# Kernel tuning notes

Measured on AMD Instinct MI355X. Metric: run time of the kernel, lower is better.

## Reference

```python
import jax, jax.numpy as jnp
import numpy as np

NUM_GRAPHS = 64
N, E, H = 100000, 3200000, 64


def _glorot(k, shape):
    fan_in = shape[0]
    return jax.random.normal(k, shape, jnp.float32) * (1.0 / np.sqrt(fan_in))


def setup_inputs() -> dict:
    key = jax.random.key(0)
    ks = jax.random.split(key, 16)
    edge_index = jax.random.randint(ks[0], (2, E), 0, N)
    edge_weight = jax.random.uniform(ks[1], (E,), dtype=jnp.float32)
    batch = jnp.sort(jax.random.randint(ks[2], (N,), 0, NUM_GRAPHS))
    return {
        "edge_index": edge_index,
        "edge_weight": edge_weight,
        "batch": batch,
        "num_nodes": N,
        "W1": _glorot(ks[3], (1, H)), "b1": jnp.zeros((H,), jnp.float32),
        "W2": _glorot(ks[4], (H, H)), "b2": jnp.zeros((H,), jnp.float32),
        "W3": _glorot(ks[5], (H, H)), "b3": jnp.zeros((H,), jnp.float32),
        "W4": _glorot(ks[6], (H, H)), "b4": jnp.zeros((H,), jnp.float32),
        "W5": _glorot(ks[7], (H, H)), "b5": jnp.zeros((H,), jnp.float32),
        "lin_w": _glorot(ks[8], (H, 1)), "lin_b": jnp.zeros((1,), jnp.float32),
    }


def _gcn_layer(x, W, b, src, dst, w, n):
    # GCNConv(normalize=False): linear transform then weighted scatter-add over edges.
    h = x @ W                                  # [N, H]
    m = h[src] * w[:, None]                    # [E, H] messages
    return jax.ops.segment_sum(m, dst, num_segments=n) + b


def reference(edge_index, edge_weight, batch, num_nodes,
              W1, b1, W2, b2, W3, b3, W4, b4, W5, b5, lin_w, lin_b):
    src, dst = edge_index[0], edge_index[1]
    x = jnp.ones((num_nodes, 1), jnp.float32)
    for W, b in ((W1, b1), (W2, b2), (W3, b3), (W4, b4), (W5, b5)):
        x = jax.nn.relu(_gcn_layer(x, W, b, src, dst, edge_weight, num_nodes))
        # dropout p=0.1 is identity in eval mode
    # global mean pool per graph
    sums = jax.ops.segment_sum(x, batch, num_segments=NUM_GRAPHS)      # [G, H]
    counts = jax.ops.segment_sum(jnp.ones((num_nodes,), x.dtype), batch,
                                 num_segments=NUM_GRAPHS)
    pooled = sums / jnp.maximum(counts, 1.0)[:, None]
    return pooled @ lin_w + lin_b                                      # [G, 1]
```

## Files before the change

kernel.cpp:

```cpp
#include <hip/hip_runtime.h>

#define H 64
#define NUM_GRAPHS 64
#define BSHIFT 8
#define BSIZE 256
#define MAXNB 512
#define CHUNK 8192
#define BKT 8192
#define PADE 16
#define CSRB (BKT + BSIZE * PADE)
#define RPB 16

typedef unsigned int uint;
typedef unsigned short ushort;
typedef __attribute__((ext_vector_type(4))) float f32x4;
typedef __attribute__((ext_vector_type(8))) short short8;

__device__ __forceinline__ float bf2f(ushort u) {
    return __uint_as_float(((uint)u) << 16);
}
__device__ __forceinline__ ushort f2bf(float f) {
    uint b = __float_as_uint(f);
    b += 0x7FFFu + ((b >> 16) & 1u);
    return (ushort)(b >> 16);
}

__global__ void init_kernel(int* __restrict__ bucketCur, int NB) {
    int i = blockIdx.x * 256 + threadIdx.x;
    if (i < NB) bucketCur[i] = i * BKT;
}

__global__ __launch_bounds__(1024) void part_kernel(const int* __restrict__ src,
        const int* __restrict__ dst, const float* __restrict__ w,
        int* __restrict__ bucketCur, int2* __restrict__ bucketed, int E, int NB) {
    __shared__ int h[MAXNB];
    __shared__ int basev[MAXNB];
    __shared__ int lbase[MAXNB + 1];
    __shared__ int s[512];
    __shared__ int2 stage[CHUNK];
    int tid = threadIdx.x;
    for (int i = tid; i < NB; i += 1024) h[i] = 0;
    __syncthreads();
    int cbase = blockIdx.x * CHUNK;
    int cend = min(cbase + CHUNK, E);
    for (int e = cbase + tid; e < cend; e += 1024)
        atomicAdd(&h[dst[e] >> BSHIFT], 1);
    __syncthreads();
    for (int i = tid; i < NB; i += 1024) {
        int c = h[i];
        basev[i] = c ? atomicAdd(&bucketCur[i], c) : 0;
    }
    if (tid < 512) s[tid] = (tid < NB) ? h[tid] : 0;
    __syncthreads();
    for (int off = 1; off < 512; off <<= 1) {
        int t = (tid < 512 && tid >= off) ? s[tid - off] : 0;
        __syncthreads();
        if (tid < 512) s[tid] += t;
        __syncthreads();
    }
    if (tid < NB) lbase[tid + 1] = s[tid];
    if (tid == 0) lbase[0] = 0;
    __syncthreads();
    for (int i = tid; i < NB; i += 1024) h[i] = 0;
    __syncthreads();
    for (int e = cbase + tid; e < cend; e += 1024) {
        int d = dst[e];
        int b = d >> BSHIFT;
        int slot = atomicAdd(&h[b], 1);
        stage[lbase[b] + slot] =
            make_int2(((d & (BSIZE - 1)) << 17) | src[e], __float_as_int(w[e]));
    }
    __syncthreads();
    int lane = tid & 63, wv = tid >> 6;
    for (int b = wv; b < NB; b += 16) {
        int lb = lbase[b], cnt = lbase[b + 1] - lb, gb = basev[b];
        int lim = (b + 1) * BKT;
        for (int k = lane; k < cnt; k += 64)
            if (gb + k < lim) bucketed[gb + k] = stage[lb + k];
    }
}

__global__ __launch_bounds__(512) void bsort_kernel(const int* __restrict__ bucketCur,
        const int2* __restrict__ bucketed, uint* __restrict__ csr,
        int2* __restrict__ rowinfo, float* __restrict__ degw, int N) {
    __shared__ int cnt[BSIZE];
    __shared__ int pos[BSIZE];
    __shared__ int cur[BSIZE];
    __shared__ float wsum[BSIZE];
    int b = blockIdx.x;
    int tid = threadIdx.x;
    int nodeBase = b << BSHIFT;
    int nNodes = min(BSIZE, N - nodeBase);
    if (tid < BSIZE) { cnt[tid] = 0; wsum[tid] = 0.f; }
    __syncthreads();
    int ebeg = b * BKT;
    int eend = min(bucketCur[b], ebeg + BKT);
    for (int e = ebeg + tid; e < eend; e += 512)
        atomicAdd(&cnt[bucketed[e].x >> 17], 1);
    __syncthreads();
    int pc = 0;
    if (tid < BSIZE) { pc = (cnt[tid] + PADE - 1) & ~(PADE - 1); pos[tid] = pc; }
    __syncthreads();
    for (int off = 1; off < BSIZE; off <<= 1) {
        int t = (tid < BSIZE && tid >= off) ? pos[tid - off] : 0;
        __syncthreads();
        if (tid < BSIZE) pos[tid] += t;
        __syncthreads();
    }
    int csrBase = b * CSRB;
    if (tid < BSIZE) {
        int excl = pos[tid] - pc;
        cur[tid] = excl;
        if (tid < nNodes) rowinfo[nodeBase + tid] = make_int2(csrBase + excl, pc);
    }
    __syncthreads();
    for (int e = ebeg + tid; e < eend; e += 512) {
        int2 v = bucketed[e];
        int dl = v.x >> 17;
        int slot = atomicAdd(&cur[dl], 1);
        uint wb = (uint)v.y;
        wb += 0x7FFFu + ((wb >> 16) & 1u);
        uint w15 = (wb >> 16) & 0x7FFFu;
        csr[csrBase + slot] = (((uint)(v.x & 0x1FFFF)) << 15) | w15;
        atomicAdd(&wsum[dl], __uint_as_float(w15 << 16));
    }
    __syncthreads();
    if (tid < nNodes) {
        degw[nodeBase + tid] = wsum[tid];
        int e0 = cur[tid];
        int e1 = pos[tid];
        for (int k = e0; k < e1; ++k) csr[csrBase + k] = 0u;
    }
}

__global__ void layer1_kernel(const float* __restrict__ degw, const float* __restrict__ W1,
                              const float* __restrict__ b1, ushort* __restrict__ out, int N) {
    int gid = blockIdx.x * 256 + threadIdx.x;
    if (gid >= N * 16) return;
    int i = gid >> 4, c4 = (gid & 15) * 4;
    float d = degw[i];
    uint lo = (uint)f2bf(fmaxf(d * W1[c4 + 0] + b1[c4 + 0], 0.f))
            | ((uint)f2bf(fmaxf(d * W1[c4 + 1] + b1[c4 + 1], 0.f)) << 16);
    uint hi = (uint)f2bf(fmaxf(d * W1[c4 + 2] + b1[c4 + 2], 0.f))
            | ((uint)f2bf(fmaxf(d * W1[c4 + 3] + b1[c4 + 3], 0.f)) << 16);
    *reinterpret_cast<uint2*>(out + ((size_t)i << 6) + c4) = make_uint2(lo, hi);
}

__global__ void count_kernel(const int* __restrict__ batch, float* __restrict__ gcnt, int N) {
    __shared__ int bins[NUM_GRAPHS];
    int tid = threadIdx.x;
    if (tid < NUM_GRAPHS) bins[tid] = 0;
    __syncthreads();
    int node = blockIdx.x * 256 + tid;
    if (node < N) atomicAdd(&bins[batch[node]], 1);
    __syncthreads();
    if (tid < NUM_GRAPHS && bins[tid])
        unsafeAtomicAdd(&gcnt[tid], (float)bins[tid]);
}

template<bool LAST>
__global__ __launch_bounds__(256) void layer_kernel(const int2* __restrict__ rowinfo,
        const uint* __restrict__ csr, const ushort* __restrict__ x,
        const float* __restrict__ W, const float* __restrict__ bvec,
        ushort* __restrict__ out, const int* __restrict__ batch,
        const float* __restrict__ linw, float* __restrict__ gsum, int N) {
    __shared__ alignas(16) ushort Wt[64][72];
    __shared__ alignas(16) ushort AG[RPB][72];
    __shared__ float gbins[NUM_GRAPHS];
    int tid = threadIdx.x;
    for (int i = tid; i < 64 * 64; i += 256) {
        int k = i >> 6, c = i & 63;
        Wt[c][k] = f2bf(W[i]);
    }
    if (LAST && tid < NUM_GRAPHS) gbins[tid] = 0.f;
    __syncthreads();
    int lane = tid & 63, wid = tid >> 6;
    int rowbase = blockIdx.x * RPB;
#pragma unroll 1
    for (int p = 0; p < 4; ++p) {
        int trow = wid * 4 + p;
        int row = rowbase + trow;
        float agg = 0.f;
        if (row < N) {
            int2 ri = rowinfo[row];
            int beg = ri.x, lenp = ri.y;
            for (int ck = 0; ck < lenp; ck += 64) {
                uint pv = 0u;
                if (ck + lane < lenp)
                    pv = __builtin_nontemporal_load(csr + beg + ck + lane);
                int ng = min(64, lenp - ck) >> 4;
                for (int g = 0; g < ng; ++g) {
                    uint ss[16]; ushort uu[16];
#pragma unroll
                    for (int j = 0; j < 16; ++j) {
                        uint s = (uint)__builtin_amdgcn_readlane((int)pv, g * 16 + j);
                        ss[j] = s;
                        uu[j] = *(x + (((size_t)(s >> 15)) << 6) + (uint)lane);
                    }
#pragma unroll
                    for (int j = 0; j < 16; ++j)
                        agg = fmaf(__uint_as_float((ss[j] & 0x7FFFu) << 16),
                                   bf2f(uu[j]), agg);
                }
            }
        }
        AG[trow][lane] = f2bf(agg);
    }
    __syncthreads();
    int cl = lane & 15, kg = lane >> 4;
    int c0 = wid * 16;
    short8 a0 = *reinterpret_cast<const short8*>(&AG[cl][kg * 8]);
    short8 a1 = *reinterpret_cast<const short8*>(&AG[cl][32 + kg * 8]);
    short8 bb0 = *reinterpret_cast<const short8*>(&Wt[c0 + cl][kg * 8]);
    short8 bb1 = *reinterpret_cast<const short8*>(&Wt[c0 + cl][32 + kg * 8]);
    f32x4 acc = {0.f, 0.f, 0.f, 0.f};
    acc = __builtin_amdgcn_mfma_f32_16x16x32_bf16(a0, bb0, acc, 0, 0, 0);
    acc = __builtin_amdgcn_mfma_f32_16x16x32_bf16(a1, bb1, acc, 0, 0, 0);
    float bias = bvec[c0 + cl];
    float lw = LAST ? linw[c0 + cl] : 0.f;
#pragma unroll
    for (int j = 0; j < 4; ++j) {
        int r = rowbase + kg * 4 + j;
        if (r < N) {
            float v = fmaxf(acc[j] + bias, 0.f);
            if (!LAST)
                __builtin_nontemporal_store(f2bf(v), out + ((size_t)r << 6) + c0 + cl);
            else
                atomicAdd(&gbins[batch[r]], v * lw);
        }
    }
    if (LAST) {
        __syncthreads();
        if (tid < NUM_GRAPHS) unsafeAtomicAdd(&gsum[tid], gbins[tid]);
    }
}

__global__ void final_kernel(const float* __restrict__ gsum, const float* __restrict__ gcnt,
                             const float* __restrict__ lin_b, float* __restrict__ out) {
    int g = threadIdx.x;
    if (g < NUM_GRAPHS) out[g] = gsum[g] / fmaxf(gcnt[g], 1.f) + lin_b[0];
}

extern "C" void kernel_launch(void* const* d_in, const int* in_sizes, int n_in,
                              void* d_out, int out_size, void* d_ws, size_t ws_size,
                              hipStream_t stream) {
    const int*   edge_index = (const int*)d_in[0];
    const float* ew    = (const float*)d_in[1];
    const int*   batch = (const int*)d_in[2];
    const float* W1    = (const float*)d_in[4];
    const float* b1    = (const float*)d_in[5];
    const float* Wl[4] = {(const float*)d_in[6], (const float*)d_in[8],
                          (const float*)d_in[10], (const float*)d_in[12]};
    const float* bl[4] = {(const float*)d_in[7], (const float*)d_in[9],
                          (const float*)d_in[11], (const float*)d_in[13]};
    const float* linw  = (const float*)d_in[14];
    const float* linb  = (const float*)d_in[15];

    const int E = in_sizes[1];
    const int N = in_sizes[2];
    const int* src = edge_index;
    const int* dst = edge_index + E;
    const int NB = (N + BSIZE - 1) >> BSHIFT;

    char* base = (char*)d_ws;
    size_t featPad = (((size_t)(N + 16) * H * 2) + 255) & ~(size_t)255;
    size_t bktBytes = (((size_t)NB * BKT * 8) + 255) & ~(size_t)255;
    size_t span = 2 * featPad > bktBytes ? 2 * featPad : bktBytes;
    ushort* bufA = (ushort*)base;
    ushort* bufB = (ushort*)(base + featPad);
    int2* bucketed = (int2*)base;
    uint* csr = (uint*)(base + span);
    size_t csrBytes = (((size_t)NB * CSRB * 4) + 255) & ~(size_t)255;
    char* tail = base + span + csrBytes;
    int2* rowinfo   = (int2*)tail;
    int* bucketCur  = (int*)(rowinfo + N);
    float* gsum     = (float*)(bucketCur + MAXNB);
    float* gcnt     = gsum + NUM_GRAPHS;
    float* degw     = gcnt + NUM_GRAPHS;

    const int chunks = (E + CHUNK - 1) / CHUNK;

    init_kernel<<<(NB + 255) / 256, 256, 0, stream>>>(bucketCur, NB);
    hipMemsetAsync(gsum, 0, 2 * NUM_GRAPHS * sizeof(float), stream);
    part_kernel<<<chunks, 1024, 0, stream>>>(src, dst, ew, bucketCur, bucketed, E, NB);
    bsort_kernel<<<NB, 512, 0, stream>>>(bucketCur, bucketed, csr, rowinfo, degw, N);

    layer1_kernel<<<(N * 16 + 255) / 256, 256, 0, stream>>>(degw, W1, b1, bufA, N);
    count_kernel<<<(N + 255) / 256, 256, 0, stream>>>(batch, gcnt, N);

    const int gridL = (N + RPB - 1) / RPB;
    ushort* xin = bufA;
    ushort* xout = bufB;
    for (int l = 0; l < 3; ++l) {
        layer_kernel<false><<<gridL, 256, 0, stream>>>(rowinfo, csr, xin, Wl[l], bl[l],
                xout, batch, linw, gsum, N);
        ushort* t = xin; xin = xout; xout = t;
    }
    layer_kernel<true><<<gridL, 256, 0, stream>>>(rowinfo, csr, xin, Wl[3], bl[3],
            xout, batch, linw, gsum, N);

    final_kernel<<<1, 64, 0, stream>>>(gsum, gcnt, linb, (float*)d_out);
}
```

Baseline: 460.5 us.

## Gather two edges per wave with 32-bit loads and prefetch next CSR chunk

Restructures the edge gather so each half-wave handles a different edge. Each lane loads a 32-bit pair of bf16 features and keeps two accumulators, and the halves are combined with a cross-lane shuffle at the end. The next 64-edge CSR chunk is prefetched while the current one is processed, and ds_bpermute replaces readlane broadcasts. Bucket padding changes from 16 to 8 and bucket capacity grows, which reduces padding work but shifts the CSR layout.

```diff
diff --git a/kernel.cpp b/kernel.cpp
--- a/kernel.cpp
+++ b/kernel.cpp
@@ -6,8 +6,8 @@
 #define BSIZE 256
 #define MAXNB 512
 #define CHUNK 8192
-#define BKT 8192
-#define PADE 16
+#define BKT 9216
+#define PADE 8
 #define CSRB (BKT + BSIZE * PADE)
 #define RPB 16
 
@@ -175,47 +175,68 @@
     if (LAST && tid < NUM_GRAPHS) gbins[tid] = 0.f;
     __syncthreads();
     int lane = tid & 63, wid = tid >> 6;
+    int half4 = (lane >> 5) << 2;
+    const char* xb = (const char*)x + (size_t)((lane & 31) << 2);
     int rowbase = blockIdx.x * RPB;
 #pragma unroll 1
     for (int p = 0; p < 4; ++p) {
         int trow = wid * 4 + p;
         int row = rowbase + trow;
-        float agg = 0.f;
+        float a0 = 0.f, a1 = 0.f;
         if (row < N) {
             int2 ri = rowinfo[row];
             int beg = ri.x, lenp = ri.y;
+            uint pv = (lane < lenp) ? __builtin_nontemporal_load(csr + beg + lane) : 0u;
+#pragma unroll 1
             for (int ck = 0; ck < lenp; ck += 64) {
-                uint pv = 0u;
-                if (ck + lane < lenp)
-                    pv = __builtin_nontemporal_load(csr + beg + ck + lane);
-                int ng = min(64, lenp - ck) >> 4;
-                for (int g = 0; g < ng; ++g) {
-                    uint ss[16]; ushort uu[16];
-#pragma unroll
-                    for (int j = 0; j < 16; ++j) {
-                        uint s = (uint)__builtin_amdgcn_readlane((int)pv, g * 16 + j);
-                        ss[j] = s;
-                        uu[j] = *(x + (((size_t)(s >> 15)) << 6) + (uint)lane);
-                    }
-#pragma unroll
-                    for (int j = 0; j < 16; ++j)
-                        agg = fmaf(__uint_as_float((ss[j] & 0x7FFFu) << 16),
-                                   bf2f(uu[j]), agg);
+                uint pvn = 0u;
+                int nidx = ck + 64 + lane;
+                if (nidx < lenp)
+                    pvn = __builtin_nontemporal_load(csr + beg + nidx);
+                int ng = min(64, lenp - ck) >> 1;
+#pragma unroll 1
+                for (int g = 0; g < ng; g += 4) {
+                    uint p0 = (uint)__builtin_amdgcn_ds_bpermute(8 * g + half4, (int)pv);
+                    uint p1 = (uint)__builtin_amdgcn_ds_bpermute(8 * g + 8 + half4, (int)pv);
+                    uint p2 = (uint)__builtin_amdgcn_ds_bpermute(8 * g + 16 + half4, (int)pv);
+                    uint p3 = (uint)__builtin_amdgcn_ds_bpermute(8 * g + 24 + half4, (int)pv);
+                    uint u0 = *reinterpret_cast<const uint*>(xb + ((size_t)(p0 >> 15) << 7));
+                    uint u1 = *reinterpret_cast<const uint*>(xb + ((size_t)(p1 >> 15) << 7));
+                    uint u2 = *reinterpret_cast<const uint*>(xb + ((size_t)(p2 >> 15) << 7));
+                    uint u3 = *reinterpret_cast<const uint*>(xb + ((size_t)(p3 >> 15) << 7));
+                    float w0 = __uint_as_float((p0 & 0x7FFFu) << 16);
+                    float w1 = __uint_as_float((p1 & 0x7FFFu) << 16);
+                    float w2 = __uint_as_float((p2 & 0x7FFFu) << 16);
+                    float w3 = __uint_as_float((p3 & 0x7FFFu) << 16);
+                    a0 = fmaf(w0, __uint_as_float(u0 << 16), a0);
+                    a1 = fmaf(w0, __uint_as_float(u0 & 0xFFFF0000u), a1);
+                    a0 = fmaf(w1, __uint_as_float(u1 << 16), a0);
+                    a1 = fmaf(w1, __uint_as_float(u1 & 0xFFFF0000u), a1);
+                    a0 = fmaf(w2, __uint_as_float(u2 << 16), a0);
+                    a1 = fmaf(w2, __uint_as_float(u2 & 0xFFFF0000u), a1);
+                    a0 = fmaf(w3, __uint_as_float(u3 << 16), a0);
+                    a1 = fmaf(w3, __uint_as_float(u3 & 0xFFFF0000u), a1);
                 }
+                pv = pvn;
             }
         }
-        AG[trow][lane] = f2bf(agg);
+        a0 += __shfl_xor(a0, 32);
+        a1 += __shfl_xor(a1, 32);
+        if (lane < 32) {
+            uint pk = (uint)f2bf(a0) | ((uint)f2bf(a1) << 16);
+            *reinterpret_cast<uint*>(&AG[trow][lane << 1]) = pk;
+        }
     }
     __syncthreads();
     int cl = lane & 15, kg = lane >> 4;
     int c0 = wid * 16;
-    short8 a0 = *reinterpret_cast<const short8*>(&AG[cl][kg * 8]);
-    short8 a1 = *reinterpret_cast<const short8*>(&AG[cl][32 + kg * 8]);
+    short8 a0v = *reinterpret_cast<const short8*>(&AG[cl][kg * 8]);
+    short8 a1v = *reinterpret_cast<const short8*>(&AG[cl][32 + kg * 8]);
     short8 bb0 = *reinterpret_cast<const short8*>(&Wt[c0 + cl][kg * 8]);
     short8 bb1 = *reinterpret_cast<const short8*>(&Wt[c0 + cl][32 + kg * 8]);
     f32x4 acc = {0.f, 0.f, 0.f, 0.f};
-    acc = __builtin_amdgcn_mfma_f32_16x16x32_bf16(a0, bb0, acc, 0, 0, 0);
-    acc = __builtin_amdgcn_mfma_f32_16x16x32_bf16(a1, bb1, acc, 0, 0, 0);
+    acc = __builtin_amdgcn_mfma_f32_16x16x32_bf16(a0v, bb0, acc, 0, 0, 0);
+    acc = __builtin_amdgcn_mfma_f32_16x16x32_bf16(a1v, bb1, acc, 0, 0, 0);
     float bias = bvec[c0 + cl];
     float lw = LAST ? linw[c0 + cl] : 0.f;
 #pragma unroll
```

Result: no change. 454.4 us (-1.3%).
